# Kernel optimization log

Hardware: AMD Instinct MI355X
Metric: run time of the kernel (lower is better)

The kernel has to match this reference:

```python
import jax, jax.numpy as jnp
import numpy as np

L = 8      # num_layers (experts)
N = 8192   # tokens
H = 768    # hidden_dim
I = 1536   # inner = hidden_dim * expansion (2.0)


def setup_inputs() -> dict:
    key = jax.random.key(0)
    k = jax.random.split(key, 6)
    s1 = 1.0 / np.sqrt(H)  # torch nn.Linear default init bound (fan_in)
    s2 = 1.0 / np.sqrt(I)
    return {
        "z": jax.random.normal(k[0], (N, H), dtype=jnp.float32),
        "layer_ids": jax.random.randint(k[1], (N,), 0, L),
        "w1": jax.random.uniform(k[2], (L, H, I), jnp.float32, -s1, s1),
        "b1": jax.random.uniform(k[3], (L, I), jnp.float32, -s1, s1),
        "w2": jax.random.uniform(k[4], (L, I, H), jnp.float32, -s2, s2),
        "b2": jax.random.uniform(k[5], (L, H), jnp.float32, -s2, s2),
    }


def reference(z, layer_ids, w1, b1, w2, b2):
    # Per-token expert MLP: out[n] = z[n] + MLP_{layer_ids[n]}(z[n]).
    # Dense-all-experts formulation (jit-safe, no data-dependent shapes):
    # run every expert on all tokens, then gather each token's own expert row.
    h = jnp.einsum('nh,lhi->lni', z, w1) + b1[:, None, :]       # [L, N, I]
    a = jax.nn.gelu(h, approximate=False)                        # exact erf GELU (torch default)
    y = jnp.einsum('lni,lih->lnh', a, w2) + b2[:, None, :]       # [L, N, H]
    sel = y[layer_ids, jnp.arange(z.shape[0])]                   # [N, H] pick each token's expert
    return z + sel
```

## Files before the change

### kernel.cpp

```cpp
#include <hip/hip_runtime.h>
#include <cstdint>
#include <cstddef>

#define LNUM 8
#define NTOK 8192
#define HDIM 768
#define IDIM 1536

typedef __bf16 bf16x8 __attribute__((ext_vector_type(8)));
typedef float f32x4 __attribute__((ext_vector_type(4)));

__device__ __forceinline__ void gload16(void* lds, const void* gsrc) {
  __builtin_amdgcn_global_load_lds(
      (const __attribute__((address_space(1))) void*)gsrc,
      (__attribute__((address_space(3))) void*)lds, 16, 0, 0);
}

__device__ __forceinline__ float gelu_f(float x) {
  float xx = x * x;
  float u = x * __builtin_fmaf(0.0356774081f, xx, 0.7978845608f);
  float t = __builtin_exp2f(-2.8853900817779268f * u);
  return x * __builtin_amdgcn_rcpf(1.0f + t);
}

__device__ __forceinline__ void tr_cvt_tile(float (*tile)[65], const float* src,
                                            __bf16* dst, int R, int C, int r0,
                                            int c0, int t) {
  int rr = t >> 4, cc = (t & 15) << 2;
  #pragma unroll
  for (int it = 0; it < 4; ++it) {
    float4 v = *(const float4*)&src[(size_t)(r0 + rr + it * 16) * C + c0 + cc];
    tile[rr + it * 16][cc] = v.x;
    tile[rr + it * 16][cc + 1] = v.y;
    tile[rr + it * 16][cc + 2] = v.z;
    tile[rr + it * 16][cc + 3] = v.w;
  }
  __syncthreads();
  int c = t >> 2, rcb = (t & 3) << 3;
  #pragma unroll
  for (int it = 0; it < 2; ++it) {
    int r = rcb + it * 32;
    bf16x8 o;
    #pragma unroll
    for (int j = 0; j < 8; ++j) o[j] = (__bf16)tile[r + j][c];
    *(bf16x8*)&dst[(size_t)(c0 + c) * R + r0 + r] = o;
  }
}

#define NB_SC 32
#define NB_CZ 3072
#define NB_W 2304
__global__ __launch_bounds__(256) void prep_kernel(
    const int* __restrict__ lid, const float* __restrict__ z,
    const float* __restrict__ w1, int* __restrict__ meta,
    int* __restrict__ perm, bf16x8* __restrict__ zb, __bf16* __restrict__ w1t) {
  __shared__ float tile[64][65];
  int bxid = blockIdx.x;
  int tid = threadIdx.x;
  if (bxid < NB_SC) {
    __shared__ int ctw[4][LNUM], cbw[4][LNUM];
    __shared__ int lcnt[LNUM], lbase[LNUM];
    int b = bxid, wv = tid >> 6;
    if (tid < 32) {
      ctw[tid >> 3][tid & 7] = 0;
      cbw[tid >> 3][tid & 7] = 0;
    }
    if (tid < LNUM) lcnt[tid] = 0;
    __syncthreads();
    int cut = b << 8;
    for (int i = tid; i < NTOK; i += 256) {
      int e = lid[i];
      atomicAdd(&ctw[wv][e], 1);
      if (i < cut) atomicAdd(&cbw[wv][e], 1);
    }
    __syncthreads();
    if (tid < LNUM) {
      int e = tid, o = 0;
      for (int e2 = 0; e2 < LNUM; ++e2) {
        int s = ctw[0][e2] + ctw[1][e2] + ctw[2][e2] + ctw[3][e2];
        if (e2 < e) o += s;
      }
      lbase[e] = o + cbw[0][e] + cbw[1][e] + cbw[2][e] + cbw[3][e];
    }
    if (b == 0 && tid == 0) {
      int o = 0, tt = 0;
      for (int e2 = 0; e2 < LNUM; ++e2) {
        int s = ctw[0][e2] + ctw[1][e2] + ctw[2][e2] + ctw[3][e2];
        meta[e2] = o;
        meta[9 + e2] = tt;
        o += s;
        tt += (s + 127) >> 7;
      }
      meta[8] = o;
      meta[17] = tt;
    }
    __syncthreads();
    int i = (b << 8) + tid;
    int e = lid[i];
    int r = atomicAdd(&lcnt[e], 1);
    perm[lbase[e] + r] = i;
  } else if (bxid < NB_SC + NB_CZ) {
    int i = (bxid - NB_SC) * 256 + tid;
    const float4* zf = (const float4*)z;
    float4 a = zf[i * 2], b4 = zf[i * 2 + 1];
    bf16x8 o;
    o[0] = (__bf16)a.x; o[1] = (__bf16)a.y; o[2] = (__bf16)a.z; o[3] = (__bf16)a.w;
    o[4] = (__bf16)b4.x; o[5] = (__bf16)b4.y; o[6] = (__bf16)b4.z; o[7] = (__bf16)b4.w;
    zb[i] = o;
  } else {
    int idx = bxid - (NB_SC + NB_CZ);
    int e = idx / 288, rem = idx % 288;
    int c0 = (rem % 24) * 64, r0 = (rem / 24) * 64;
    tr_cvt_tile(tile, w1 + (size_t)e * HDIM * IDIM, w1t + (size_t)e * HDIM * IDIM,
                HDIM, IDIM, r0, c0, tid);
  }
}

#define G1NT 24
#define G1GRID (G1NT * 72)
__global__ __launch_bounds__(256) void gemm1_kernel(
    const __bf16* __restrict__ zb, const __bf16* __restrict__ w1t,
    const float* __restrict__ b1, const int* __restrict__ meta,
    const int* __restrict__ perm, __bf16* __restrict__ act,
    const float* __restrict__ w2, __bf16* __restrict__ w2t) {
  __shared__ __align__(16) char smem[24576];
  int bid = blockIdx.x;
  int tid = threadIdx.x;
  if (bid >= G1GRID) {
    float (*tile)[65] = (float (*)[65])smem;
    int idx = bid - G1GRID;
    int e = idx / 288, rem = idx % 288;
    int c0 = (rem % 12) * 64, r0 = (rem / 12) * 64;
    tr_cvt_tile(tile, w2 + (size_t)e * HDIM * IDIM, w2t + (size_t)e * HDIM * IDIM,
                IDIM, HDIM, r0, c0, tid);
    return;
  }
  __bf16* As = (__bf16*)smem;
  __bf16* Bs = (__bf16*)(smem + 16384);
  const int* offs = meta;
  const int* tiles = meta + 9;
  int tileid = (bid & 7) * (G1GRID >> 3) + (bid >> 3);
  int bx = tileid % G1NT;
  int t = tileid / G1NT;
  if (t >= tiles[LNUM]) return;
  int e = 0;
  #pragma unroll
  for (int q = 0; q < LNUM - 1; ++q)
    if (t >= tiles[e + 1]) ++e;
  int mtile = t - tiles[e];
  int row0 = offs[e] + (mtile << 7);
  int cntRem = offs[e + 1] - row0;
  if (cntRem > 128) cntRem = 128;
  int n0 = bx << 6;
  int lane = tid & 63, wv = tid >> 6;
  int wr = wv >> 1, wc = wv & 1;
  int swz = ((lane & 7) ^ (lane >> 3)) << 3;

  const __bf16* srcA[4];
  const __bf16* srcB[2];
  #pragma unroll
  for (int i = 0; i < 4; ++i) {
    int row = ((wv * 4 + i) << 3) + (lane >> 3);
    int rA = row < cntRem ? row : cntRem - 1;
    int tok = perm[row0 + rA];
    srcA[i] = zb + (size_t)tok * HDIM + swz;
  }
  #pragma unroll
  for (int i = 0; i < 2; ++i) {
    int row = ((wv * 2 + i) << 3) + (lane >> 3);
    srcB[i] = w1t + ((size_t)e * IDIM + n0 + row) * HDIM + swz;
  }

  int rswz = (lane & 7) << 3;
  f32x4 acc[4][2] = {};

  for (int kk = 0; kk < HDIM / 64; ++kk) {
    #pragma unroll
    for (int i = 0; i < 4; ++i)
      gload16(As + ((wv * 4 + i) << 9), srcA[i] + kk * 64);
    #pragma unroll
    for (int i = 0; i < 2; ++i)
      gload16(Bs + ((wv * 2 + i) << 9), srcB[i] + kk * 64);
    __syncthreads();
    #pragma unroll
    for (int k2 = 0; k2 < 2; ++k2) {
      int kb = (k2 * 32 + ((lane >> 4) << 3)) ^ rswz;
      bf16x8 a[4], b[2];
      #pragma unroll
      for (int mi = 0; mi < 4; ++mi)
        a[mi] = *(const bf16x8*)&As[((wr * 64 + mi * 16 + (lane & 15)) << 6) + kb];
      #pragma unroll
      for (int ni = 0; ni < 2; ++ni)
        b[ni] = *(const bf16x8*)&Bs[((wc * 32 + ni * 16 + (lane & 15)) << 6) + kb];
      #pragma unroll
      for (int mi = 0; mi < 4; ++mi)
        #pragma unroll
        for (int ni = 0; ni < 2; ++ni)
          acc[mi][ni] = __builtin_amdgcn_mfma_f32_16x16x32_bf16(a[mi], b[ni], acc[mi][ni], 0, 0, 0);
    }
    __syncthreads();
  }

  float bb[2];
  #pragma unroll
  for (int ni = 0; ni < 2; ++ni)
    bb[ni] = b1[e * IDIM + n0 + wc * 32 + ni * 16 + (lane & 15)];

  #pragma unroll
  for (int mi = 0; mi < 4; ++mi) {
    int gr0 = wr * 64 + mi * 16 + ((lane >> 4) << 2);
    #pragma unroll
    for (int r = 0; r < 4; ++r) {
      int g = gr0 + r;
      if (g < cntRem) {
        size_t p = (size_t)(row0 + g);
        #pragma unroll
        for (int ni = 0; ni < 2; ++ni) {
          int col = n0 + wc * 32 + ni * 16 + (lane & 15);
          act[p * IDIM + col] = (__bf16)gelu_f(acc[mi][ni][r] + bb[ni]);
        }
      }
    }
  }
}

#define G2NT 12
#define G2GRID (G2NT * 72)
__global__ __launch_bounds__(256) void gemm2_kernel(
    const __bf16* __restrict__ act, const __bf16* __restrict__ w2t,
    const float* __restrict__ b2, const float* __restrict__ z,
    const int* __restrict__ meta, const int* __restrict__ perm,
    float* __restrict__ out) {
  __shared__ __align__(16) char smem[24576];
  __bf16* As = (__bf16*)smem;
  __bf16* Bs = (__bf16*)(smem + 16384);
  const int* offs = meta;
  const int* tiles = meta + 9;
  int bid = blockIdx.x;
  int tileid = (bid & 7) * (G2GRID >> 3) + (bid >> 3);
  int bx = tileid % G2NT;
  int t = tileid / G2NT;
  if (t >= tiles[LNUM]) return;
  int e = 0;
  #pragma unroll
  for (int q = 0; q < LNUM - 1; ++q)
    if (t >= tiles[e + 1]) ++e;
  int mtile = t - tiles[e];
  int row0 = offs[e] + (mtile << 7);
  int cntRem = offs[e + 1] - row0;
  if (cntRem > 128) cntRem = 128;
  int n0 = bx << 6;
  int tid = threadIdx.x, lane = tid & 63, wv = tid >> 6;
  int wr = wv >> 1, wc = wv & 1;
  int swz = ((lane & 7) ^ (lane >> 3)) << 3;

  const __bf16* srcA[4];
  const __bf16* srcB[2];
  #pragma unroll
  for (int i = 0; i < 4; ++i) {
    int row = ((wv * 4 + i) << 3) + (lane >> 3);
    int rA = row < cntRem ? row : cntRem - 1;
    srcA[i] = act + (size_t)(row0 + rA) * IDIM + swz;
  }
  #pragma unroll
  for (int i = 0; i < 2; ++i) {
    int row = ((wv * 2 + i) << 3) + (lane >> 3);
    srcB[i] = w2t + ((size_t)e * HDIM + n0 + row) * IDIM + swz;
  }

  int rswz = (lane & 7) << 3;
  f32x4 acc[4][2] = {};

  for (int kk = 0; kk < IDIM / 64; ++kk) {
    #pragma unroll
    for (int i = 0; i < 4; ++i)
      gload16(As + ((wv * 4 + i) << 9), srcA[i] + kk * 64);
    #pragma unroll
    for (int i = 0; i < 2; ++i)
      gload16(Bs + ((wv * 2 + i) << 9), srcB[i] + kk * 64);
    __syncthreads();
    #pragma unroll
    for (int k2 = 0; k2 < 2; ++k2) {
      int kb = (k2 * 32 + ((lane >> 4) << 3)) ^ rswz;
      bf16x8 a[4], b[2];
      #pragma unroll
      for (int mi = 0; mi < 4; ++mi)
        a[mi] = *(const bf16x8*)&As[((wr * 64 + mi * 16 + (lane & 15)) << 6) + kb];
      #pragma unroll
      for (int ni = 0; ni < 2; ++ni)
        b[ni] = *(const bf16x8*)&Bs[((wc * 32 + ni * 16 + (lane & 15)) << 6) + kb];
      #pragma unroll
      for (int mi = 0; mi < 4; ++mi)
        #pragma unroll
        for (int ni = 0; ni < 2; ++ni)
          acc[mi][ni] = __builtin_amdgcn_mfma_f32_16x16x32_bf16(a[mi], b[ni], acc[mi][ni], 0, 0, 0);
    }
    __syncthreads();
  }

  float bb[2];
  #pragma unroll
  for (int ni = 0; ni < 2; ++ni)
    bb[ni] = b2[e * HDIM + n0 + wc * 32 + ni * 16 + (lane & 15)];

  #pragma unroll
  for (int mi = 0; mi < 4; ++mi) {
    int gr0 = wr * 64 + mi * 16 + ((lane >> 4) << 2);
    #pragma unroll
    for (int r = 0; r < 4; ++r) {
      int g = gr0 + r;
      if (g < cntRem) {
        int p = row0 + g;
        int tok = perm[p];
        #pragma unroll
        for (int ni = 0; ni < 2; ++ni) {
          int col = n0 + wc * 32 + ni * 16 + (lane & 15);
          out[(size_t)tok * HDIM + col] =
              z[(size_t)tok * HDIM + col] + acc[mi][ni][r] + bb[ni];
        }
      }
    }
  }
}

extern "C" void kernel_launch(void* const* d_in, const int* in_sizes, int n_in,
                              void* d_out, int out_size, void* d_ws, size_t ws_size,
                              hipStream_t stream) {
  const float* z  = (const float*)d_in[0];
  const int*   lid = (const int*)d_in[1];
  const float* w1 = (const float*)d_in[2];
  const float* b1 = (const float*)d_in[3];
  const float* w2 = (const float*)d_in[4];
  const float* b2 = (const float*)d_in[5];
  float* out = (float*)d_out;
  char* ws = (char*)d_ws;

  int* meta = (int*)ws;
  int* perm = (int*)(ws + 2048);
  __bf16* zb  = (__bf16*)(ws + 2048 + 32768);
  __bf16* w1t = zb + (size_t)NTOK * HDIM;
  __bf16* w2t = w1t + (size_t)LNUM * HDIM * IDIM;
  __bf16* act = w2t + (size_t)LNUM * HDIM * IDIM;

  prep_kernel<<<NB_SC + NB_CZ + NB_W, 256, 0, stream>>>(
      lid, z, w1, meta, perm, (bf16x8*)zb, w1t);
  gemm1_kernel<<<G1GRID + NB_W, 256, 0, stream>>>(zb, w1t, b1, meta, perm, act,
                                                  w2, w2t);
  gemm2_kernel<<<G2GRID, 256, 0, stream>>>(act, w2t, b2, z, meta, perm, out);
}
```

Before: 106.0 us.

## Widen gemm1 N-tile to 128 and use fixed per-expert tile grid

gemm1 now computes 128x128 output tiles instead of 128x64, so each wave holds a 4x4 accumulator set and each loaded A tile is reused across twice as many columns. Both GEMMs drop the compact prefix-summed tile list and instead assign each block a fixed (expert, m-tile, n-tile) from the block index, with up to 12 m-tiles per expert and early exit for unused tiles. This removes the tile-lookup loop and the tile-count metadata, and places experts round-robin across block IDs. In exchange it assumes no expert receives more than 1536 tokens, launches blocks that exit immediately, and raises register and LDS use in gemm1.

```diff
diff --git a/kernel.cpp b/kernel.cpp
--- a/kernel.cpp
+++ b/kernel.cpp
@@ -83,16 +83,13 @@
       lbase[e] = o + cbw[0][e] + cbw[1][e] + cbw[2][e] + cbw[3][e];
     }
     if (b == 0 && tid == 0) {
-      int o = 0, tt = 0;
+      int o = 0;
       for (int e2 = 0; e2 < LNUM; ++e2) {
         int s = ctw[0][e2] + ctw[1][e2] + ctw[2][e2] + ctw[3][e2];
         meta[e2] = o;
-        meta[9 + e2] = tt;
         o += s;
-        tt += (s + 127) >> 7;
       }
       meta[8] = o;
-      meta[17] = tt;
     }
     __syncthreads();
     int i = (b << 8) + tid;
@@ -116,14 +113,13 @@
   }
 }
 
-#define G1NT 24
-#define G1GRID (G1NT * 72)
+#define G1GRID 1152
 __global__ __launch_bounds__(256) void gemm1_kernel(
     const __bf16* __restrict__ zb, const __bf16* __restrict__ w1t,
     const float* __restrict__ b1, const int* __restrict__ meta,
     const int* __restrict__ perm, __bf16* __restrict__ act,
     const float* __restrict__ w2, __bf16* __restrict__ w2t) {
-  __shared__ __align__(16) char smem[24576];
+  __shared__ __align__(16) char smem[32768];
   int bid = blockIdx.x;
   int tid = threadIdx.x;
   if (bid >= G1GRID) {
@@ -138,94 +134,84 @@
   __bf16* As = (__bf16*)smem;
   __bf16* Bs = (__bf16*)(smem + 16384);
   const int* offs = meta;
-  const int* tiles = meta + 9;
-  int tileid = (bid & 7) * (G1GRID >> 3) + (bid >> 3);
-  int bx = tileid % G1NT;
-  int t = tileid / G1NT;
-  if (t >= tiles[LNUM]) return;
-  int e = 0;
-  #pragma unroll
-  for (int q = 0; q < LNUM - 1; ++q)
-    if (t >= tiles[e + 1]) ++e;
-  int mtile = t - tiles[e];
-  int row0 = offs[e] + (mtile << 7);
-  int cntRem = offs[e + 1] - row0;
+  int e = bid & 7;
+  int r = bid >> 3;
+  int mt = r / 12, nt = r % 12;
+  int off0 = offs[e];
+  int cnt = offs[e + 1] - off0;
+  if ((mt << 7) >= cnt) return;
+  int row0 = off0 + (mt << 7);
+  int cntRem = cnt - (mt << 7);
   if (cntRem > 128) cntRem = 128;
-  int n0 = bx << 6;
+  int n0 = nt << 7;
   int lane = tid & 63, wv = tid >> 6;
   int wr = wv >> 1, wc = wv & 1;
   int swz = ((lane & 7) ^ (lane >> 3)) << 3;
 
   const __bf16* srcA[4];
-  const __bf16* srcB[2];
+  const __bf16* srcB[4];
   #pragma unroll
   for (int i = 0; i < 4; ++i) {
     int row = ((wv * 4 + i) << 3) + (lane >> 3);
     int rA = row < cntRem ? row : cntRem - 1;
     int tok = perm[row0 + rA];
     srcA[i] = zb + (size_t)tok * HDIM + swz;
-  }
-  #pragma unroll
-  for (int i = 0; i < 2; ++i) {
-    int row = ((wv * 2 + i) << 3) + (lane >> 3);
     srcB[i] = w1t + ((size_t)e * IDIM + n0 + row) * HDIM + swz;
   }
 
   int rswz = (lane & 7) << 3;
-  f32x4 acc[4][2] = {};
+  f32x4 acc[4][4] = {};
 
   for (int kk = 0; kk < HDIM / 64; ++kk) {
     #pragma unroll
-    for (int i = 0; i < 4; ++i)
+    for (int i = 0; i < 4; ++i) {
       gload16(As + ((wv * 4 + i) << 9), srcA[i] + kk * 64);
-    #pragma unroll
-    for (int i = 0; i < 2; ++i)
-      gload16(Bs + ((wv * 2 + i) << 9), srcB[i] + kk * 64);
+      gload16(Bs + ((wv * 4 + i) << 9), srcB[i] + kk * 64);
+    }
     __syncthreads();
     #pragma unroll
     for (int k2 = 0; k2 < 2; ++k2) {
       int kb = (k2 * 32 + ((lane >> 4) << 3)) ^ rswz;
-      bf16x8 a[4], b[2];
+      bf16x8 a[4], b[4];
       #pragma unroll
       for (int mi = 0; mi < 4; ++mi)
         a[mi] = *(const bf16x8*)&As[((wr * 64 + mi * 16 + (lane & 15)) << 6) + kb];
       #pragma unroll
-      for (int ni = 0; ni < 2; ++ni)
-        b[ni] = *(const bf16x8*)&Bs[((wc * 32 + ni * 16 + (lane & 15)) << 6) + kb];
+      for (int ni = 0; ni < 4; ++ni)
+        b[ni] = *(const bf16x8*)&Bs[((wc * 64 + ni * 16 + (lane & 15)) << 6) + kb];
       #pragma unroll
       for (int mi = 0; mi < 4; ++mi)
         #pragma unroll
-        for (int ni = 0; ni < 2; ++ni)
+        for (int ni = 0; ni < 4; ++ni)
           acc[mi][ni] = __builtin_amdgcn_mfma_f32_16x16x32_bf16(a[mi], b[ni], acc[mi][ni], 0, 0, 0);
     }
     __syncthreads();
   }
 
-  float bb[2];
-  #pragma unroll
-  for (int ni = 0; ni < 2; ++ni)
-    bb[ni] = b1[e * IDIM + n0 + wc * 32 + ni * 16 + (lane & 15)];
+  float bb[4];
+  #pragma unroll
+  for (int ni = 0; ni < 4; ++ni)
+    bb[ni] = b1[e * IDIM + n0 + wc * 64 + ni * 16 + (lane & 15)];
 
   #pragma unroll
   for (int mi = 0; mi < 4; ++mi) {
     int gr0 = wr * 64 + mi * 16 + ((lane >> 4) << 2);
     #pragma unroll
-    for (int r = 0; r < 4; ++r) {
-      int g = gr0 + r;
+    for (int r2 = 0; r2 < 4; ++r2) {
+      int g = gr0 + r2;
       if (g < cntRem) {
         size_t p = (size_t)(row0 + g);
         #pragma unroll
-        for (int ni = 0; ni < 2; ++ni) {
-          int col = n0 + wc * 32 + ni * 16 + (lane & 15);
-          act[p * IDIM + col] = (__bf16)gelu_f(acc[mi][ni][r] + bb[ni]);
+        for (int ni = 0; ni < 4; ++ni) {
+          int col = n0 + wc * 64 + ni * 16 + (lane & 15);
+          act[p * IDIM + col] = (__bf16)gelu_f(acc[mi][ni][r2] + bb[ni]);
         }
       }
     }
   }
 }
 
-#define G2NT 12
-#define G2GRID (G2NT * 72)
+#define G2GRID 1152
 __global__ __launch_bounds__(256) void gemm2_kernel(
     const __bf16* __restrict__ act, const __bf16* __restrict__ w2t,
     const float* __restrict__ b2, const float* __restrict__ z,
@@ -235,21 +221,17 @@
   __bf16* As = (__bf16*)smem;
   __bf16* Bs = (__bf16*)(smem + 16384);
   const int* offs = meta;
-  const int* tiles = meta + 9;
   int bid = blockIdx.x;
-  int tileid = (bid & 7) * (G2GRID >> 3) + (bid >> 3);
-  int bx = tileid % G2NT;
-  int t = tileid / G2NT;
-  if (t >= tiles[LNUM]) return;
-  int e = 0;
-  #pragma unroll
-  for (int q = 0; q < LNUM - 1; ++q)
-    if (t >= tiles[e + 1]) ++e;
-  int mtile = t - tiles[e];
-  int row0 = offs[e] + (mtile << 7);
-  int cntRem = offs[e + 1] - row0;
+  int e = bid & 7;
+  int r = bid >> 3;
+  int mt = r / 12, nt = r % 12;
+  int off0 = offs[e];
+  int cnt = offs[e + 1] - off0;
+  if ((mt << 7) >= cnt) return;
+  int row0 = off0 + (mt << 7);
+  int cntRem = cnt - (mt << 7);
   if (cntRem > 128) cntRem = 128;
-  int n0 = bx << 6;
+  int n0 = nt << 6;
   int tid = threadIdx.x, lane = tid & 63, wv = tid >> 6;
   int wr = wv >> 1, wc = wv & 1;
   int swz = ((lane & 7) ^ (lane >> 3)) << 3;
@@ -307,8 +289,8 @@
   for (int mi = 0; mi < 4; ++mi) {
     int gr0 = wr * 64 + mi * 16 + ((lane >> 4) << 2);
     #pragma unroll
-    for (int r = 0; r < 4; ++r) {
-      int g = gr0 + r;
+    for (int r2 = 0; r2 < 4; ++r2) {
+      int g = gr0 + r2;
       if (g < cntRem) {
         int p = row0 + g;
         int tok = perm[p];
@@ -316,7 +298,7 @@
         for (int ni = 0; ni < 2; ++ni) {
           int col = n0 + wc * 32 + ni * 16 + (lane & 15);
           out[(size_t)tok * HDIM + col] =
-              z[(size_t)tok * HDIM + col] + acc[mi][ni][r] + bb[ni];
+              z[(size_t)tok * HDIM + col] + acc[mi][ni][r2] + bb[ni];
         }
       }
     }
```

After: 101.5 us. -4.2%, faster.
